# Performance work log

Hardware: AMD Instinct MI355X
Metric: run time of the kernel (lower is better)

The kernel has to match this reference:

```python
import jax, jax.numpy as jnp
import numpy as np

B, S, E, H = 8, 2048, 1024, 64  # batch, seq (== block_size), emb_size, head_size


def setup_inputs() -> dict:
    key = jax.random.key(0)
    ks = jax.random.split(key, 7)
    s = 1.0 / np.sqrt(E)  # ~ torch Linear default init scale
    return {
        "x": jax.random.normal(ks[0], (B, S, E), dtype=jnp.float32),
        "Wk": jax.random.uniform(ks[1], (H, E), jnp.float32, -s, s),
        "bk": jax.random.uniform(ks[2], (H,), jnp.float32, -s, s),
        "Wq": jax.random.uniform(ks[3], (H, E), jnp.float32, -s, s),
        "bq": jax.random.uniform(ks[4], (H,), jnp.float32, -s, s),
        "Wv": jax.random.uniform(ks[5], (H, E), jnp.float32, -s, s),
        "bv": jax.random.uniform(ks[6], (H,), jnp.float32, -s, s),
    }


def reference(x, Wk, bk, Wq, bq, Wv, bv):
    # Linear projections (torch Linear: y = x @ W.T + b)
    xk = jnp.einsum('bse,he->bsh', x, Wk) + bk  # [B,S,H]
    xq = jnp.einsum('bse,he->bsh', x, Wq) + bq
    xv = jnp.einsum('bse,he->bsh', x, Wv) + bv
    # raw scores q @ k^T  -> [B,S,S]
    wei = jnp.einsum('bqh,bkh->bqk', xq, xk)
    # causal mask (encoder=True branch in source; tril==0 -> -inf)
    causal = jnp.tril(jnp.ones((x.shape[1], x.shape[1]), dtype=bool))
    wei = jnp.where(causal, wei, -jnp.inf)
    # NOTE: source divides by head_size**(-0.5), i.e. MULTIPLIES by sqrt(head_size)
    scale = jnp.asarray(Wk.shape[0], jnp.float32) ** 0.5
    wei = jax.nn.softmax(wei * scale, axis=-1)
    return jnp.einsum('bqk,bkh->bqh', wei, xv)
```

## Files before the change

kernel.cpp:

```cpp
#include <hip/hip_runtime.h>

typedef _Float16 f16;
typedef _Float16 f16x8 __attribute__((ext_vector_type(8)));
typedef _Float16 f16x4 __attribute__((ext_vector_type(4)));
typedef float f32x4 __attribute__((ext_vector_type(4)));

#define MFMA16(a, b, c) __builtin_amdgcn_mfma_f32_16x16x32_f16(a, b, c, 0, 0, 0)

constexpr int Bn = 8, Sn = 2048, En = 1024, Hn = 64;
constexpr int Mn = Bn * Sn;
constexpr float QSCALE = 11.5415603f;
constexpr float THR = 11.5f;

__device__ __forceinline__ void gload_lds16(const void* g, void* lds) {
    __builtin_amdgcn_global_load_lds(
        (const __attribute__((address_space(1))) void*)g,
        (__attribute__((address_space(3))) void*)lds, 16, 0, 0);
}
__device__ __forceinline__ void wait_vm4() {
    asm volatile("s_waitcnt vmcnt(4)" ::: "memory");
    __builtin_amdgcn_sched_barrier(0);
}
__device__ __forceinline__ void wait_vm0() {
    asm volatile("s_waitcnt vmcnt(0)" ::: "memory");
    __builtin_amdgcn_sched_barrier(0);
}
__device__ __forceinline__ void barrier_raw() {
    __builtin_amdgcn_s_barrier();
    __builtin_amdgcn_sched_barrier(0);
}

__global__ __launch_bounds__(256) void convw_kernel(
    const float* __restrict__ Wq, const float* __restrict__ Wk,
    const float* __restrict__ Wv, f16* __restrict__ Wc)
{
    const int h = blockIdx.x * 256 + threadIdx.x;
    const int kt = h / 1536;
    const int rem = h - kt * 1536;
    const int rr = rem >> 3;
    const int c = rem & 7;
    const int set = rr >> 6;
    const float* src = (set == 0 ? Wq : (set == 1 ? Wk : Wv))
                       + (size_t)(rr & 63) * En + kt * 64 + c * 8;
    float4 v0 = *reinterpret_cast<const float4*>(src);
    float4 v1 = *reinterpret_cast<const float4*>(src + 4);
    f16x8 o = {(f16)v0.x, (f16)v0.y, (f16)v0.z, (f16)v0.w,
               (f16)v1.x, (f16)v1.y, (f16)v1.z, (f16)v1.w};
    const int cs = c ^ (rr & 7);
    *reinterpret_cast<f16x8*>(Wc + (size_t)kt * 12288 + rr * 64 + cs * 8) = o;
}

__global__ __launch_bounds__(512) void proj_kernel(
    const float* __restrict__ x, const f16* __restrict__ Wc,
    const float* __restrict__ bq, const float* __restrict__ bk,
    const float* __restrict__ bv,
    f16* __restrict__ qws, f16* __restrict__ kws, f16* __restrict__ vtws)
{
    __shared__ __align__(16) char ldsb[2 * 32768];
    const int tid = threadIdx.x;
    const int w = tid >> 6, l = tid & 63;
    const int l15 = l & 15, lhi = l >> 4;
    const int rt = w & 1, nh = w >> 1;
    const int Mbase = blockIdx.x * 32;

    f32x4 acc[3];
#pragma unroll
    for (int i = 0; i < 3; ++i) acc[i] = (f32x4){0.f, 0.f, 0.f, 0.f};

    const int xr_s = w * 4 + (l >> 4);
    const int xc_s = (l & 15) ^ (xr_s & 7);

#define WSTAGE(buf, kb)                                                       \
    {                                                                         \
        const f16* wt_ = Wc + (size_t)(kb) * 12288;                           \
        _Pragma("unroll")                                                     \
        for (int r_ = 0; r_ < 3; ++r_)                                        \
            gload_lds16(wt_ + r_ * 4096 + w * 512 + l * 8,                    \
                        ldsb + (buf) * 32768 + r_ * 8192 + w * 1024);         \
    }

#define XSTAGE(buf, kb)                                                       \
    {                                                                         \
        const float* xs_ = x + (size_t)(Mbase + xr_s) * En + (kb) * 64        \
                           + xc_s * 4;                                        \
        gload_lds16(xs_, ldsb + (buf) * 32768 + 24576 + w * 1024);            \
    }

#define COMPUTE(buf)                                                          \
    {                                                                         \
        const int xrow_ = rt * 16 + l15;                                      \
        const char* xb_ = ldsb + (buf) * 32768 + 24576 + xrow_ * 256;         \
        f16x8 a_[2];                                                          \
        _Pragma("unroll")                                                     \
        for (int kc_ = 0; kc_ < 2; ++kc_) {                                   \
            const int c0_ = kc_ * 8 + lhi * 2;                                \
            float4 lo_ = *reinterpret_cast<const float4*>(                    \
                xb_ + ((c0_ ^ (l15 & 7)) * 16));                              \
            float4 hi_ = *reinterpret_cast<const float4*>(                    \
                xb_ + (((c0_ + 1) ^ (l15 & 7)) * 16));                        \
            a_[kc_] = (f16x8){(f16)lo_.x, (f16)lo_.y, (f16)lo_.z, (f16)lo_.w, \
                              (f16)hi_.x, (f16)hi_.y, (f16)hi_.z, (f16)hi_.w};\
        }                                                                     \
        _Pragma("unroll")                                                     \
        for (int i_ = 0; i_ < 3; ++i_) {                                      \
            const int row16_ = (nh * 3 + i_) * 16 + l15;                      \
            _Pragma("unroll")                                                 \
            for (int kc_ = 0; kc_ < 2; ++kc_) {                               \
                const int addr_ = (buf) * 32768 + row16_ * 128                \
                    + ((kc_ * 64 + lhi * 16) ^ ((l15 & 7) << 4));             \
                f16x8 b_ = *reinterpret_cast<const f16x8*>(ldsb + addr_);     \
                acc[i_] = MFMA16(a_[kc_], b_, acc[i_]);                       \
            }                                                                 \
        }                                                                     \
    }

    WSTAGE(0, 0);
    XSTAGE(0, 0);
#pragma unroll
    for (int i = 0; i < 16; ++i) {
        const int cur = i & 1;
        if (i < 15) {
            WSTAGE(cur ^ 1, i + 1);
            XSTAGE(cur ^ 1, i + 1);
            wait_vm4();
        } else {
            wait_vm0();
        }
        barrier_raw();
        COMPUTE(cur);
        barrier_raw();
    }
#undef WSTAGE
#undef XSTAGE
#undef COMPUTE

    const int batch = Mbase >> 11;
    const int r0 = Mbase + rt * 16 + lhi * 4;
#pragma unroll
    for (int i = 0; i < 3; ++i) {
        const int nt = nh * 3 + i;
        const int set = nt >> 2;
        const int h = (nt & 3) * 16 + l15;
        const float bias = (set == 0 ? bq : (set == 1 ? bk : bv))[h];
        if (set == 0) {
#pragma unroll
            for (int r = 0; r < 4; ++r)
                qws[(size_t)(r0 + r) * Hn + h] =
                    (f16)((acc[i][r] + bias) * QSCALE);
        } else if (set == 1) {
#pragma unroll
            for (int r = 0; r < 4; ++r)
                kws[(size_t)(r0 + r) * Hn + h] = (f16)(acc[i][r] + bias);
        } else {
            const int s0v = r0 & (Sn - 1);
            const int sp = (s0v & ~31) + ((s0v & 12) << 1)
                         + ((s0v & 16) ? 4 : 0);
            f16x4 hv = {(f16)(acc[i][0] + bias), (f16)(acc[i][1] + bias),
                        (f16)(acc[i][2] + bias), (f16)(acc[i][3] + bias)};
            *reinterpret_cast<f16x4*>(
                &vtws[(size_t)batch * Hn * Sn + (size_t)h * Sn + sp]) = hv;
        }
    }
}

__global__ __launch_bounds__(256, 3) void attn_kernel(
    const f16* __restrict__ qws, const f16* __restrict__ kws,
    const f16* __restrict__ vtws, float* __restrict__ out,
    float* __restrict__ slots)
{
    const int tid = threadIdx.x;
    const int w = tid >> 6, l = tid & 63;
    const int l15 = l & 15, lhi = l >> 4;

    const int L = blockIdx.x * 4 + w;
    const int u = (int)(((unsigned)L * 997u) % 2304u);
    const int b = u / 288;
    const int t = u - b * 288;
    int k = 0;
#pragma unroll
    for (int gg = 1; gg < 8; ++gg)
        if (t >= 4 * gg * (gg + 1)) k = gg;
    const int rem = t - 4 * k * (k + 1);
    const int jq = rem / (k + 1);
    const int c = rem - jq * (k + 1);
    const int J = 8 * k + jq;

    const int qbase = J * 32;
    const int nkt = J + 1;
    const int ts = c * 8;
    const int te = (ts + 8 < nkt) ? ts + 8 : nkt;
    const bool hasDiag = (te == nkt);
    const int nfull = te - (hasDiag ? 1 : 0);

    const f16* qb = qws + (size_t)b * Sn * Hn;
    const f16* kb = kws + (size_t)b * Sn * Hn;
    const f16* vtb = vtws + (size_t)b * Hn * Sn;

    f16x8 qf[2][2];
#pragma unroll
    for (int rs = 0; rs < 2; ++rs)
#pragma unroll
        for (int kc = 0; kc < 2; ++kc)
            qf[rs][kc] = *reinterpret_cast<const f16x8*>(
                &qb[(size_t)(qbase + rs * 16 + l15) * Hn + kc * 32 + lhi * 8]);

    f32x4 O[2][4];
#pragma unroll
    for (int rs = 0; rs < 2; ++rs)
#pragma unroll
        for (int nt = 0; nt < 4; ++nt) O[rs][nt] = (f32x4){0.f, 0.f, 0.f, 0.f};
    float m1[2] = {-1e30f, -1e30f}, l1[2] = {0.f, 0.f};

#define ATTN_ITER(KT, MASKED)                                                 \
    {                                                                         \
        const int kbase = (KT) * 32;                                          \
        f16x8 kf[2][2];                                                       \
        _Pragma("unroll") for (int nt = 0; nt < 2; ++nt)                      \
        _Pragma("unroll") for (int kc = 0; kc < 2; ++kc)                      \
            kf[nt][kc] = *reinterpret_cast<const f16x8*>(                     \
                &kb[(size_t)(kbase + nt * 16 + l15) * Hn + kc * 32            \
                    + lhi * 8]);                                              \
        f32x4 Sv[2][2];                                                       \
        _Pragma("unroll") for (int rs = 0; rs < 2; ++rs)                      \
        _Pragma("unroll") for (int nt = 0; nt < 2; ++nt) {                    \
            f32x4 sa = (f32x4){0.f, 0.f, 0.f, 0.f};                           \
            sa = MFMA16(kf[nt][0], qf[rs][0], sa);                            \
            sa = MFMA16(kf[nt][1], qf[rs][1], sa);                            \
            Sv[rs][nt] = sa;                                                  \
        }                                                                     \
        float tv[2][2][4];                                                    \
        float mx[2];                                                          \
        _Pragma("unroll") for (int rs = 0; rs < 2; ++rs) {                    \
            _Pragma("unroll") for (int nt = 0; nt < 2; ++nt)                  \
            _Pragma("unroll") for (int r = 0; r < 4; ++r) {                   \
                float v = Sv[rs][nt][r];                                      \
                if (MASKED) {                                                 \
                    const int key_ = nt * 16 + lhi * 4 + r;                   \
                    const int qq_ = rs * 16 + l15;                            \
                    v = (key_ <= qq_) ? v : -1e30f;                           \
                }                                                             \
                tv[rs][nt][r] = v;                                            \
            }                                                                 \
            float a0 = fmaxf(fmaxf(tv[rs][0][0], tv[rs][0][1]),               \
                             fmaxf(tv[rs][0][2], tv[rs][0][3]));              \
            float a1 = fmaxf(fmaxf(tv[rs][1][0], tv[rs][1][1]),               \
                             fmaxf(tv[rs][1][2], tv[rs][1][3]));              \
            float m_ = fmaxf(a0, a1);                                         \
            m_ = fmaxf(m_, __shfl_xor(m_, 16));                               \
            m_ = fmaxf(m_, __shfl_xor(m_, 32));                               \
            mx[rs] = m_;                                                      \
        }                                                                     \
        const int need = (mx[0] > m1[0] + THR) || (mx[1] > m1[1] + THR);      \
        if (__any(need)) {                                                    \
            _Pragma("unroll") for (int rs = 0; rs < 2; ++rs) {                \
                const float mn = fmaxf(m1[rs], mx[rs]);                       \
                const float al = exp2f(m1[rs] - mn);                          \
                l1[rs] *= al;                                                 \
                _Pragma("unroll") for (int nt = 0; nt < 4; ++nt)              \
                _Pragma("unroll") for (int r = 0; r < 4; ++r)                 \
                    O[rs][nt][r] *= al;                                       \
                m1[rs] = mn;                                                  \
            }                                                                 \
        }                                                                     \
        f16x8 pa[2];                                                          \
        _Pragma("unroll") for (int rs = 0; rs < 2; ++rs) {                    \
            float p_[8];                                                      \
            float s_ = 0.f;                                                   \
            _Pragma("unroll") for (int nt = 0; nt < 2; ++nt)                  \
            _Pragma("unroll") for (int r = 0; r < 4; ++r) {                   \
                const float e_ = exp2f(tv[rs][nt][r] - m1[rs]);               \
                p_[nt * 4 + r] = e_;                                          \
                s_ += e_;                                                     \
            }                                                                 \
            s_ += __shfl_xor(s_, 16);                                         \
            s_ += __shfl_xor(s_, 32);                                         \
            l1[rs] += s_;                                                     \
            pa[rs] = (f16x8){(f16)p_[0], (f16)p_[1], (f16)p_[2], (f16)p_[3],  \
                             (f16)p_[4], (f16)p_[5], (f16)p_[6], (f16)p_[7]}; \
        }                                                                     \
        _Pragma("unroll") for (int nt = 0; nt < 4; ++nt) {                    \
            f16x8 vf = *reinterpret_cast<const f16x8*>(                       \
                &vtb[(size_t)(nt * 16 + l15) * Sn + kbase + lhi * 8]);        \
            O[0][nt] = MFMA16(vf, pa[0], O[0][nt]);                           \
            O[1][nt] = MFMA16(vf, pa[1], O[1][nt]);                           \
        }                                                                     \
    }

    for (int kt = ts; kt < nfull; ++kt) ATTN_ITER(kt, false);
    if (hasDiag) ATTN_ITER(J, true);
#undef ATTN_ITER

    if (J < 8) {
#pragma unroll
        for (int rs = 0; rs < 2; ++rs) {
            const float inv = 1.0f / l1[rs];
            const size_t ro = ((size_t)b * Sn + qbase + rs * 16 + l15) * Hn;
#pragma unroll
            for (int nt = 0; nt < 4; ++nt) {
                float4 o = {O[rs][nt][0] * inv, O[rs][nt][1] * inv,
                            O[rs][nt][2] * inv, O[rs][nt][3] * inv};
                *reinterpret_cast<float4*>(&out[ro + nt * 16 + lhi * 4]) = o;
            }
        }
    } else {
        float* sl = slots + (size_t)(b * 280 + 4 * k * (k + 1) - 8
                                     + jq * (k + 1) + c) * 1088;
        f16* so = reinterpret_cast<f16*>(sl + 64);
#pragma unroll
        for (int rs = 0; rs < 2; ++rs) {
            const int row = rs * 16 + l15;
            const float inv = 1.0f / l1[rs];
            if (lhi == 0) { sl[row] = m1[rs]; sl[32 + row] = l1[rs]; }
#pragma unroll
            for (int nt = 0; nt < 4; ++nt) {
                f16x4 hv = {(f16)(O[rs][nt][0] * inv), (f16)(O[rs][nt][1] * inv),
                            (f16)(O[rs][nt][2] * inv), (f16)(O[rs][nt][3] * inv)};
                *reinterpret_cast<f16x4*>(
                    &so[row * 64 + nt * 16 + lhi * 4]) = hv;
            }
        }
    }
}

__global__ __launch_bounds__(256) void comb_kernel(
    const float* __restrict__ slots, float* __restrict__ out)
{
    const int id = blockIdx.x;
    const int b = id / 56, jj = id - b * 56;
    const int J = 8 + jj;
    const int k = J >> 3;
    const int nch = k + 1;
    const float* base = slots + (size_t)(b * 280 + 4 * k * (k + 1) - 8
                                         + (J - 8 * k) * (k + 1)) * 1088;
    const int tid = threadIdx.x;
    const int row = tid >> 3;
    const int h0 = (tid & 7) * 8;

    float mg = -1e30f;
    for (int cc = 0; cc < nch; ++cc)
        mg = fmaxf(mg, base[cc * 1088 + row]);
    float den = 0.f;
    float num[8] = {0.f, 0.f, 0.f, 0.f, 0.f, 0.f, 0.f, 0.f};
    for (int cc = 0; cc < nch; ++cc) {
        const float* sl = base + cc * 1088;
        const float wgt = sl[32 + row] * exp2f(sl[row] - mg);
        den += wgt;
        const f16* so = reinterpret_cast<const f16*>(sl + 64);
        f16x8 ov = *reinterpret_cast<const f16x8*>(&so[row * 64 + h0]);
#pragma unroll
        for (int i = 0; i < 8; ++i) num[i] += (float)ov[i] * wgt;
    }
    const float inv = 1.0f / den;
    const size_t ro = ((size_t)b * Sn + J * 32 + row) * Hn + h0;
    float4 o0 = {num[0] * inv, num[1] * inv, num[2] * inv, num[3] * inv};
    float4 o1 = {num[4] * inv, num[5] * inv, num[6] * inv, num[7] * inv};
    *reinterpret_cast<float4*>(&out[ro]) = o0;
    *reinterpret_cast<float4*>(&out[ro + 4]) = o1;
}

extern "C" void kernel_launch(void* const* d_in, const int* in_sizes, int n_in,
                              void* d_out, int out_size, void* d_ws, size_t ws_size,
                              hipStream_t stream) {
    const float* x  = (const float*)d_in[0];
    const float* Wk = (const float*)d_in[1];
    const float* bk = (const float*)d_in[2];
    const float* Wq = (const float*)d_in[3];
    const float* bq = (const float*)d_in[4];
    const float* Wv = (const float*)d_in[5];
    const float* bv = (const float*)d_in[6];

    f16* qws  = (f16*)d_ws;
    f16* kws  = qws + (size_t)Mn * Hn;
    f16* vtws = kws + (size_t)Mn * Hn;
    f16* Wc   = vtws + (size_t)Mn * Hn;
    float* slots = (float*)(Wc + 196608);

    convw_kernel<<<96, 256, 0, stream>>>(Wq, Wk, Wv, Wc);
    proj_kernel<<<512, 512, 0, stream>>>(x, Wc, bq, bk, bv, qws, kws, vtws);
    attn_kernel<<<576, 256, 0, stream>>>(qws, kws, vtws, (float*)d_out, slots);
    comb_kernel<<<448, 256, 0, stream>>>(slots, (float*)d_out);
}
```

Baseline: 61.09 us.

## Double projection M-tile, halve attention KV chunk size, use packed fp16 conversions

The projection kernel now gives each block 64 rows instead of 32, so every wave computes two 16-row subtiles that share the weight fragments loaded from LDS. This halves the number of weight reloads per row and enlarges LDS, with the wait count adjusted for the extra x load. The attention split-K work decomposition goes from 8 to 4 key tiles per chunk, doubling attention blocks (1088) for better load balance, at the cost of more partial slots for the combine kernel. Scalar float-to-half conversions are replaced with packed round-toward-zero cvt_pkrtz, which changes rounding slightly.

Measured after the change: 68.83 us. +12.7%, slower.

```diff
diff --git a/kernel.cpp b/kernel.cpp
--- a/kernel.cpp
+++ b/kernel.cpp
@@ -3,6 +3,7 @@
 typedef _Float16 f16;
 typedef _Float16 f16x8 __attribute__((ext_vector_type(8)));
 typedef _Float16 f16x4 __attribute__((ext_vector_type(4)));
+typedef __fp16 fp16x2 __attribute__((ext_vector_type(2)));
 typedef float f32x4 __attribute__((ext_vector_type(4)));
 
 #define MFMA16(a, b, c) __builtin_amdgcn_mfma_f32_16x16x32_f16(a, b, c, 0, 0, 0)
@@ -17,8 +18,8 @@
         (const __attribute__((address_space(1))) void*)g,
         (__attribute__((address_space(3))) void*)lds, 16, 0, 0);
 }
-__device__ __forceinline__ void wait_vm4() {
-    asm volatile("s_waitcnt vmcnt(4)" ::: "memory");
+__device__ __forceinline__ void wait_vm5() {
+    asm volatile("s_waitcnt vmcnt(5)" ::: "memory");
     __builtin_amdgcn_sched_barrier(0);
 }
 __device__ __forceinline__ void wait_vm0() {
@@ -28,6 +29,14 @@
 __device__ __forceinline__ void barrier_raw() {
     __builtin_amdgcn_s_barrier();
     __builtin_amdgcn_sched_barrier(0);
+}
+__device__ __forceinline__ f16x8 cvt8(float4 lo, float4 hi) {
+    union { f16x8 v; fp16x2 h[4]; } u;
+    u.h[0] = __builtin_amdgcn_cvt_pkrtz(lo.x, lo.y);
+    u.h[1] = __builtin_amdgcn_cvt_pkrtz(lo.z, lo.w);
+    u.h[2] = __builtin_amdgcn_cvt_pkrtz(hi.x, hi.y);
+    u.h[3] = __builtin_amdgcn_cvt_pkrtz(hi.z, hi.w);
+    return u.v;
 }
 
 __global__ __launch_bounds__(256) void convw_kernel(
@@ -44,8 +53,7 @@
                        + (size_t)(rr & 63) * En + kt * 64 + c * 8;
     float4 v0 = *reinterpret_cast<const float4*>(src);
     float4 v1 = *reinterpret_cast<const float4*>(src + 4);
-    f16x8 o = {(f16)v0.x, (f16)v0.y, (f16)v0.z, (f16)v0.w,
-               (f16)v1.x, (f16)v1.y, (f16)v1.z, (f16)v1.w};
+    f16x8 o = cvt8(v0, v1);
     const int cs = c ^ (rr & 7);
     *reinterpret_cast<f16x8*>(Wc + (size_t)kt * 12288 + rr * 64 + cs * 8) = o;
 }
@@ -56,19 +64,19 @@
     const float* __restrict__ bv,
     f16* __restrict__ qws, f16* __restrict__ kws, f16* __restrict__ vtws)
 {
-    __shared__ __align__(16) char ldsb[2 * 32768];
+    __shared__ __align__(16) char ldsb[2 * 40960];
     const int tid = threadIdx.x;
     const int w = tid >> 6, l = tid & 63;
     const int l15 = l & 15, lhi = l >> 4;
-    const int rt = w & 1, nh = w >> 1;
-    const int Mbase = blockIdx.x * 32;
-
-    f32x4 acc[3];
-#pragma unroll
-    for (int i = 0; i < 3; ++i) acc[i] = (f32x4){0.f, 0.f, 0.f, 0.f};
-
-    const int xr_s = w * 4 + (l >> 4);
-    const int xc_s = (l & 15) ^ (xr_s & 7);
+    const int mh = w & 1, nh = w >> 1;
+    const int Mbase = blockIdx.x * 64;
+
+    f32x4 acc[6];
+#pragma unroll
+    for (int i = 0; i < 6; ++i) acc[i] = (f32x4){0.f, 0.f, 0.f, 0.f};
+
+    const int xr0 = w * 4 + (l >> 4);
+    const int xc  = l & 15;
 
 #define WSTAGE(buf, kb)                                                       \
     {                                                                         \
@@ -76,40 +84,48 @@
         _Pragma("unroll")                                                     \
         for (int r_ = 0; r_ < 3; ++r_)                                        \
             gload_lds16(wt_ + r_ * 4096 + w * 512 + l * 8,                    \
-                        ldsb + (buf) * 32768 + r_ * 8192 + w * 1024);         \
+                        ldsb + (buf) * 40960 + r_ * 8192 + w * 1024);         \
     }
 
 #define XSTAGE(buf, kb)                                                       \
     {                                                                         \
-        const float* xs_ = x + (size_t)(Mbase + xr_s) * En + (kb) * 64        \
-                           + xc_s * 4;                                        \
-        gload_lds16(xs_, ldsb + (buf) * 32768 + 24576 + w * 1024);            \
+        _Pragma("unroll")                                                     \
+        for (int e_ = 0; e_ < 2; ++e_) {                                      \
+            const int r_ = e_ * 32 + xr0;                                     \
+            const float* xs_ = x + (size_t)(Mbase + r_) * En + (kb) * 64      \
+                               + (xc ^ (r_ & 7)) * 4;                         \
+            gload_lds16(xs_, ldsb + (buf) * 40960 + 24576                     \
+                             + (e_ * 8 + w) * 1024);                          \
+        }                                                                     \
     }
 
 #define COMPUTE(buf)                                                          \
     {                                                                         \
-        const int xrow_ = rt * 16 + l15;                                      \
-        const char* xb_ = ldsb + (buf) * 32768 + 24576 + xrow_ * 256;         \
-        f16x8 a_[2];                                                          \
+        f16x8 a_[2][2];                                                       \
         _Pragma("unroll")                                                     \
-        for (int kc_ = 0; kc_ < 2; ++kc_) {                                   \
-            const int c0_ = kc_ * 8 + lhi * 2;                                \
-            float4 lo_ = *reinterpret_cast<const float4*>(                    \
-                xb_ + ((c0_ ^ (l15 & 7)) * 16));                              \
-            float4 hi_ = *reinterpret_cast<const float4*>(                    \
-                xb_ + (((c0_ + 1) ^ (l15 & 7)) * 16));                        \
-            a_[kc_] = (f16x8){(f16)lo_.x, (f16)lo_.y, (f16)lo_.z, (f16)lo_.w, \
-                              (f16)hi_.x, (f16)hi_.y, (f16)hi_.z, (f16)hi_.w};\
+        for (int sub_ = 0; sub_ < 2; ++sub_) {                                \
+            const int xrow_ = mh * 32 + sub_ * 16 + l15;                      \
+            const char* xb_ = ldsb + (buf) * 40960 + 24576 + xrow_ * 256;     \
+            _Pragma("unroll")                                                 \
+            for (int kc_ = 0; kc_ < 2; ++kc_) {                               \
+                const int c0_ = kc_ * 8 + lhi * 2;                            \
+                float4 lo_ = *reinterpret_cast<const float4*>(                \
+                    xb_ + ((c0_ ^ (xrow_ & 7)) * 16));                        \
+                float4 hi_ = *reinterpret_cast<const float4*>(                \
+                    xb_ + (((c0_ + 1) ^ (xrow_ & 7)) * 16));                  \
+                a_[sub_][kc_] = cvt8(lo_, hi_);                               \
+            }                                                                 \
         }                                                                     \
         _Pragma("unroll")                                                     \
         for (int i_ = 0; i_ < 3; ++i_) {                                      \
             const int row16_ = (nh * 3 + i_) * 16 + l15;                      \
             _Pragma("unroll")                                                 \
             for (int kc_ = 0; kc_ < 2; ++kc_) {                               \
-                const int addr_ = (buf) * 32768 + row16_ * 128                \
+                const int addr_ = (buf) * 40960 + row16_ * 128                \
                     + ((kc_ * 64 + lhi * 16) ^ ((l15 & 7) << 4));             \
                 f16x8 b_ = *reinterpret_cast<const f16x8*>(ldsb + addr_);     \
-                acc[i_] = MFMA16(a_[kc_], b_, acc[i_]);                       \
+                acc[i_] = MFMA16(a_[0][kc_], b_, acc[i_]);                    \
+                acc[3 + i_] = MFMA16(a_[1][kc_], b_, acc[3 + i_]);            \
             }                                                                 \
         }                                                                     \
     }
@@ -122,7 +138,7 @@
         if (i < 15) {
             WSTAGE(cur ^ 1, i + 1);
             XSTAGE(cur ^ 1, i + 1);
-            wait_vm4();
+            wait_vm5();
         } else {
             wait_vm0();
         }
@@ -135,30 +151,34 @@
 #undef COMPUTE
 
     const int batch = Mbase >> 11;
-    const int r0 = Mbase + rt * 16 + lhi * 4;
-#pragma unroll
-    for (int i = 0; i < 3; ++i) {
-        const int nt = nh * 3 + i;
-        const int set = nt >> 2;
-        const int h = (nt & 3) * 16 + l15;
-        const float bias = (set == 0 ? bq : (set == 1 ? bk : bv))[h];
-        if (set == 0) {
-#pragma unroll
-            for (int r = 0; r < 4; ++r)
-                qws[(size_t)(r0 + r) * Hn + h] =
-                    (f16)((acc[i][r] + bias) * QSCALE);
-        } else if (set == 1) {
-#pragma unroll
-            for (int r = 0; r < 4; ++r)
-                kws[(size_t)(r0 + r) * Hn + h] = (f16)(acc[i][r] + bias);
-        } else {
-            const int s0v = r0 & (Sn - 1);
-            const int sp = (s0v & ~31) + ((s0v & 12) << 1)
-                         + ((s0v & 16) ? 4 : 0);
-            f16x4 hv = {(f16)(acc[i][0] + bias), (f16)(acc[i][1] + bias),
-                        (f16)(acc[i][2] + bias), (f16)(acc[i][3] + bias)};
-            *reinterpret_cast<f16x4*>(
-                &vtws[(size_t)batch * Hn * Sn + (size_t)h * Sn + sp]) = hv;
+#pragma unroll
+    for (int sub = 0; sub < 2; ++sub) {
+        const int r0 = Mbase + mh * 32 + sub * 16 + lhi * 4;
+#pragma unroll
+        for (int i = 0; i < 3; ++i) {
+            const int nt = nh * 3 + i;
+            const int set = nt >> 2;
+            const int h = (nt & 3) * 16 + l15;
+            const float bias = (set == 0 ? bq : (set == 1 ? bk : bv))[h];
+            const f32x4 a = acc[sub * 3 + i];
+            if (set == 0) {
+#pragma unroll
+                for (int r = 0; r < 4; ++r)
+                    qws[(size_t)(r0 + r) * Hn + h] =
+                        (f16)((a[r] + bias) * QSCALE);
+            } else if (set == 1) {
+#pragma unroll
+                for (int r = 0; r < 4; ++r)
+                    kws[(size_t)(r0 + r) * Hn + h] = (f16)(a[r] + bias);
+            } else {
+                const int s0v = r0 & (Sn - 1);
+                const int sp = (s0v & ~31) + ((s0v & 12) << 1)
+                             + ((s0v & 16) ? 4 : 0);
+                f16x4 hv = {(f16)(a[0] + bias), (f16)(a[1] + bias),
+                            (f16)(a[2] + bias), (f16)(a[3] + bias)};
+                *reinterpret_cast<f16x4*>(
+                    &vtws[(size_t)batch * Hn * Sn + (size_t)h * Sn + sp]) = hv;
+            }
         }
     }
 }
@@ -173,22 +193,22 @@
     const int l15 = l & 15, lhi = l >> 4;
 
     const int L = blockIdx.x * 4 + w;
-    const int u = (int)(((unsigned)L * 997u) % 2304u);
-    const int b = u / 288;
-    const int t = u - b * 288;
-    int k = 0;
-#pragma unroll
-    for (int gg = 1; gg < 8; ++gg)
-        if (t >= 4 * gg * (gg + 1)) k = gg;
-    const int rem = t - 4 * k * (k + 1);
-    const int jq = rem / (k + 1);
-    const int c = rem - jq * (k + 1);
-    const int J = 8 * k + jq;
+    const int u = (int)(((unsigned)L * 997u) % 4352u);
+    const int b = u / 544;
+    const int t = u - b * 544;
+    int g = 0;
+#pragma unroll
+    for (int gg = 1; gg < 16; ++gg)
+        if (t >= 2 * gg * (gg + 1)) g = gg;
+    const int rem = t - 2 * g * (g + 1);
+    const int jq = rem / (g + 1);
+    const int c = rem - jq * (g + 1);
+    const int J = 4 * g + jq;
 
     const int qbase = J * 32;
     const int nkt = J + 1;
-    const int ts = c * 8;
-    const int te = (ts + 8 < nkt) ? ts + 8 : nkt;
+    const int ts = c * 4;
+    const int te = (ts + 4 < nkt) ? ts + 4 : nkt;
     const bool hasDiag = (te == nkt);
     const int nfull = te - (hasDiag ? 1 : 0);
 
@@ -275,8 +295,8 @@
             s_ += __shfl_xor(s_, 16);                                         \
             s_ += __shfl_xor(s_, 32);                                         \
             l1[rs] += s_;                                                     \
-            pa[rs] = (f16x8){(f16)p_[0], (f16)p_[1], (f16)p_[2], (f16)p_[3],  \
-                             (f16)p_[4], (f16)p_[5], (f16)p_[6], (f16)p_[7]}; \
+            pa[rs] = cvt8((float4){p_[0], p_[1], p_[2], p_[3]},               \
+                          (float4){p_[4], p_[5], p_[6], p_[7]});              \
         }                                                                     \
         _Pragma("unroll") for (int nt = 0; nt < 4; ++nt) {                    \
             f16x8 vf = *reinterpret_cast<const f16x8*>(                       \
@@ -290,7 +310,7 @@
     if (hasDiag) ATTN_ITER(J, true);
 #undef ATTN_ITER
 
-    if (J < 8) {
+    if (J < 4) {
 #pragma unroll
         for (int rs = 0; rs < 2; ++rs) {
             const float inv = 1.0f / l1[rs];
@@ -303,8 +323,8 @@
             }
         }
     } else {
-        float* sl = slots + (size_t)(b * 280 + 4 * k * (k + 1) - 8
-                                     + jq * (k + 1) + c) * 1088;
+        float* sl = slots + (size_t)(b * 540 + 2 * g * (g + 1) - 4
+                                     + jq * (g + 1) + c) * 1088;
         f16* so = reinterpret_cast<f16*>(sl + 64);
 #pragma unroll
         for (int rs = 0; rs < 2; ++rs) {
@@ -326,12 +346,12 @@
     const float* __restrict__ slots, float* __restrict__ out)
 {
     const int id = blockIdx.x;
-    const int b = id / 56, jj = id - b * 56;
-    const int J = 8 + jj;
-    const int k = J >> 3;
-    const int nch = k + 1;
-    const float* base = slots + (size_t)(b * 280 + 4 * k * (k + 1) - 8
-                                         + (J - 8 * k) * (k + 1)) * 1088;
+    const int b = id / 60, jj = id - b * 60;
+    const int J = 4 + jj;
+    const int g = J >> 2;
+    const int nch = g + 1;
+    const float* base = slots + (size_t)(b * 540 + 2 * g * (g + 1) - 4
+                                         + (J - 4 * g) * (g + 1)) * 1088;
     const int tid = threadIdx.x;
     const int row = tid >> 3;
     const int h0 = (tid & 7) * 8;
@@ -376,7 +396,7 @@
     float* slots = (float*)(Wc + 196608);
 
     convw_kernel<<<96, 256, 0, stream>>>(Wq, Wk, Wv, Wc);
-    proj_kernel<<<512, 512, 0, stream>>>(x, Wc, bq, bk, bv, qws, kws, vtws);
-    attn_kernel<<<576, 256, 0, stream>>>(qws, kws, vtws, (float*)d_out, slots);
-    comb_kernel<<<448, 256, 0, stream>>>(slots, (float*)d_out);
-}
+    proj_kernel<<<256, 512, 0, stream>>>(x, Wc, bq, bk, bv, qws, kws, vtws);
+    attn_kernel<<<1088, 256, 0, stream>>>(qws, kws, vtws, (float*)d_out, slots);
+    comb_kernel<<<480, 256, 0, stream>>>(slots, (float*)d_out);
+}
```
